# Kernel optimization log

Hardware: AMD Instinct MI355X
Metric: run time of the kernel (lower is better)

Reference implementation:

```python
import jax, jax.numpy as jnp
import numpy as np

N_HEADS = 16

def setup_inputs() -> dict:
    key = jax.random.key(0)
    k0, k1, k2 = jax.random.split(key, 3)
    B, T, C = 4, 2048, 1024
    x = jax.random.normal(k0, (B, T, C), dtype=jnp.float32)
    # nn.Linear params: y = x @ W.T + b
    w_qkv = jax.random.normal(k1, (3 * C, C), dtype=jnp.float32) * 0.02
    b_qkv = jnp.zeros((3 * C,), dtype=jnp.float32)
    w_proj = jax.random.normal(k2, (C, C), dtype=jnp.float32) * 0.02
    b_proj = jnp.zeros((C,), dtype=jnp.float32)
    return {"x": x, "w_qkv": w_qkv, "b_qkv": b_qkv, "w_proj": w_proj, "b_proj": b_proj}

def reference(x, w_qkv, b_qkv, w_proj, b_proj):
    B, T, C = x.shape
    H = N_HEADS
    hd = C // H
    qkv = x @ w_qkv.T + b_qkv                      # [B, T, 3C]
    q, k, v = jnp.split(qkv, 3, axis=-1)           # each [B, T, C]
    q = q.reshape(B, T, H, hd).transpose(0, 2, 1, 3)  # [B, H, T, hd]
    k = k.reshape(B, T, H, hd).transpose(0, 2, 1, 3)
    v = v.reshape(B, T, H, hd).transpose(0, 2, 1, 3)
    # note: original scales by emb_dim**-0.5 (C), not head_dim**-0.5
    wei = jnp.einsum("bhqd,bhkd->bhqk", q, k) * (C ** -0.5)  # [B, H, T, T]
    causal = jnp.tril(jnp.ones((T, T), dtype=bool))
    wei = jnp.where(causal, wei, -jnp.inf)
    att = jax.nn.softmax(wei, axis=-1)
    out = jnp.einsum("bhqk,bhkd->bhqd", att, v)    # [B, H, T, hd]
    out = out.transpose(0, 2, 1, 3).reshape(B, T, C)
    return out @ w_proj.T + b_proj
```

## Files before the change

### kernel.cpp

```cpp
#include <hip/hip_runtime.h>
#include <hip/hip_bf16.h>

typedef __bf16 bf16;
typedef __bf16 bf16x8 __attribute__((ext_vector_type(8)));
typedef __bf16 bf16x4 __attribute__((ext_vector_type(4)));
typedef float  f32x4  __attribute__((ext_vector_type(4)));

#define LDS_ASYNC16(g, l)                                            \
  __builtin_amdgcn_global_load_lds(                                  \
      (const __attribute__((address_space(1))) void*)(g),            \
      (__attribute__((address_space(3))) void*)(l), 16, 0, 0)

#define QSCALE 0.04508421995f

__global__ void cvt3_f32_bf16(const float* __restrict__ i0, bf16* __restrict__ o0, int n0,
                              const float* __restrict__ i1, bf16* __restrict__ o1, int n1,
                              const float* __restrict__ i2, bf16* __restrict__ o2, int n2) {
  int i = blockIdx.x * blockDim.x + threadIdx.x;
  const float* in;
  bf16* out;
  if (i < n0) {
    in = i0; out = o0;
  } else if (i < n0 + n1) {
    i -= n0; in = i1; out = o1;
  } else {
    i -= n0 + n1;
    if (i >= n2) return;
    in = i2; out = o2;
  }
  float4 v = ((const float4*)in)[i];
  bf16x4 o = {(bf16)v.x, (bf16)v.y, (bf16)v.z, (bf16)v.w};
  ((bf16x4*)out)[i] = o;
}

template <int MODE>
__global__ __launch_bounds__(512, 1) void gemm_bt(
    const bf16* __restrict__ A, const bf16* __restrict__ B,
    const float* __restrict__ bias, float* __restrict__ outf,
    bf16* __restrict__ oq, bf16* __restrict__ ok, bf16* __restrict__ ov,
    int M, int N, int K) {
  __shared__ __align__(16) bf16 As[2][256 * 64];
  __shared__ __align__(16) bf16 Bs[2][256 * 64];
  const int tid = threadIdx.x;
  const int wave = tid >> 6, lane = tid & 63;
  const int quad = lane >> 4, l15 = lane & 15, l7 = l15 & 7;
  const int wm = wave >> 2, wn = wave & 3;
  const int bm = blockIdx.x * 256, bn = blockIdx.y * 256;

  f32x4 acc[8][4] = {};

  const int csw = ((tid & 7) ^ ((tid >> 3) & 7)) * 8;
  const bf16* gA = A + (size_t)(bm + (tid >> 3)) * K + csw;
  const bf16* gB = B + (size_t)(bn + (tid >> 3)) * K + csw;
  const int KT = K >> 6;

#define ST_A(kt, cb, rb)                                               \
  LDS_ASYNC16(gA + (size_t)(rb) * K + (size_t)(kt) * 64,               \
              (char*)As + (cb) * 32768 + (rb) * 128 + wave * 1024)
#define ST_B(kt, cb, rb)                                               \
  LDS_ASYNC16(gB + (size_t)(rb) * K + (size_t)(kt) * 64,               \
              (char*)Bs + (cb) * 32768 + (rb) * 128 + wave * 1024)

  ST_A(0, 0, 0);   ST_A(0, 0, 128);
  ST_B(0, 0, 0);   ST_B(0, 0, 64);
  ST_A(0, 0, 64);  ST_A(0, 0, 192);
  ST_B(0, 0, 128); ST_B(0, 0, 192);
  ST_A(1, 1, 0);   ST_A(1, 1, 128);
  ST_B(1, 1, 0);   ST_B(1, 1, 64);
  ST_A(1, 1, 64);  ST_A(1, 1, 192);
  asm volatile("s_waitcnt vmcnt(6)" ::: "memory");
  __builtin_amdgcn_sched_barrier(0);
  __builtin_amdgcn_s_barrier();
  __builtin_amdgcn_sched_barrier(0);

  const int rowA = wm * 128 + l15;
  const int rowB = wn * 64 + l15;
  const int c0 = (quad ^ l7) * 16, c1 = ((4 + quad) ^ l7) * 16;

#pragma unroll 1
  for (int kt = 0; kt < KT; ++kt) {
    const int c = kt & 1;
    const char* bA = (const char*)As + c * 32768;
    const char* bB = (const char*)Bs + c * 32768;
    bf16x8 af[4][2], bg0[2][2], bg1[2][2];

#pragma unroll
    for (int mi = 0; mi < 4; ++mi) {
      af[mi][0] = *(const bf16x8*)(bA + (rowA + mi * 16) * 128 + c0);
      af[mi][1] = *(const bf16x8*)(bA + (rowA + mi * 16) * 128 + c1);
    }
#pragma unroll
    for (int ni = 0; ni < 2; ++ni) {
      bg0[ni][0] = *(const bf16x8*)(bB + (rowB + ni * 16) * 128 + c0);
      bg0[ni][1] = *(const bf16x8*)(bB + (rowB + ni * 16) * 128 + c1);
    }
    if (kt + 1 < KT) { ST_B(kt + 1, c ^ 1, 128); ST_B(kt + 1, c ^ 1, 192); }
    __builtin_amdgcn_sched_barrier(0);
    __builtin_amdgcn_s_barrier();
    asm volatile("s_waitcnt lgkmcnt(0)" ::: "memory");
    __builtin_amdgcn_sched_barrier(0);
    __builtin_amdgcn_s_setprio(1);
#pragma unroll
    for (int s = 0; s < 2; ++s)
#pragma unroll
      for (int mi = 0; mi < 4; ++mi)
#pragma unroll
        for (int ni = 0; ni < 2; ++ni)
          acc[mi][ni] = __builtin_amdgcn_mfma_f32_16x16x32_bf16(
              af[mi][s], bg0[ni][s], acc[mi][ni], 0, 0, 0);
    __builtin_amdgcn_s_setprio(0);
    __builtin_amdgcn_sched_barrier(0);
    __builtin_amdgcn_s_barrier();

#pragma unroll
    for (int ni = 0; ni < 2; ++ni) {
      bg1[ni][0] = *(const bf16x8*)(bB + (rowB + 32 + ni * 16) * 128 + c0);
      bg1[ni][1] = *(const bf16x8*)(bB + (rowB + 32 + ni * 16) * 128 + c1);
    }
    if (kt + 2 < KT) { ST_A(kt + 2, c, 0); ST_A(kt + 2, c, 128); }
    __builtin_amdgcn_sched_barrier(0);
    __builtin_amdgcn_s_barrier();
    asm volatile("s_waitcnt lgkmcnt(0)" ::: "memory");
    __builtin_amdgcn_sched_barrier(0);
    __builtin_amdgcn_s_setprio(1);
#pragma unroll
    for (int s = 0; s < 2; ++s)
#pragma unroll
      for (int mi = 0; mi < 4; ++mi)
#pragma unroll
        for (int ni = 0; ni < 2; ++ni)
          acc[mi][ni + 2] = __builtin_amdgcn_mfma_f32_16x16x32_bf16(
              af[mi][s], bg1[ni][s], acc[mi][ni + 2], 0, 0, 0);
    __builtin_amdgcn_s_setprio(0);
    __builtin_amdgcn_sched_barrier(0);
    __builtin_amdgcn_s_barrier();

#pragma unroll
    for (int mi = 0; mi < 4; ++mi) {
      af[mi][0] = *(const bf16x8*)(bA + (rowA + 64 + mi * 16) * 128 + c0);
      af[mi][1] = *(const bf16x8*)(bA + (rowA + 64 + mi * 16) * 128 + c1);
    }
    if (kt + 2 < KT) { ST_B(kt + 2, c, 0); ST_B(kt + 2, c, 64); }
    __builtin_amdgcn_sched_barrier(0);
    __builtin_amdgcn_s_barrier();
    asm volatile("s_waitcnt lgkmcnt(0)" ::: "memory");
    __builtin_amdgcn_sched_barrier(0);
    __builtin_amdgcn_s_setprio(1);
#pragma unroll
    for (int s = 0; s < 2; ++s)
#pragma unroll
      for (int mi = 0; mi < 4; ++mi)
#pragma unroll
        for (int ni = 0; ni < 2; ++ni)
          acc[mi + 4][ni + 2] = __builtin_amdgcn_mfma_f32_16x16x32_bf16(
              af[mi][s], bg1[ni][s], acc[mi + 4][ni + 2], 0, 0, 0);
    __builtin_amdgcn_s_setprio(0);
    __builtin_amdgcn_sched_barrier(0);
    __builtin_amdgcn_s_barrier();

    if (kt + 2 < KT) { ST_A(kt + 2, c, 64); ST_A(kt + 2, c, 192); }
    __builtin_amdgcn_sched_barrier(0);
    __builtin_amdgcn_s_barrier();
    __builtin_amdgcn_sched_barrier(0);
    __builtin_amdgcn_s_setprio(1);
#pragma unroll
    for (int s = 0; s < 2; ++s)
#pragma unroll
      for (int mi = 0; mi < 4; ++mi)
#pragma unroll
        for (int ni = 0; ni < 2; ++ni)
          acc[mi + 4][ni] = __builtin_amdgcn_mfma_f32_16x16x32_bf16(
              af[mi][s], bg0[ni][s], acc[mi + 4][ni], 0, 0, 0);
    __builtin_amdgcn_s_setprio(0);
    __builtin_amdgcn_sched_barrier(0);
    if (kt + 1 < KT) {
      if (kt + 2 < KT)
        asm volatile("s_waitcnt vmcnt(6)" ::: "memory");
      else
        asm volatile("s_waitcnt vmcnt(0)" ::: "memory");
      __builtin_amdgcn_sched_barrier(0);
      __builtin_amdgcn_s_barrier();
      __builtin_amdgcn_sched_barrier(0);
    }
  }
#undef ST_A
#undef ST_B

#pragma unroll
  for (int mi = 0; mi < 8; ++mi) {
    const int row0 = bm + wm * 128 + mi * 16 + quad * 4;
#pragma unroll
    for (int ni = 0; ni < 4; ++ni) {
      const int col = bn + wn * 64 + ni * 16 + l15;
      const float bv = bias[col];
      if (MODE == 0) {
#pragma unroll
        for (int r = 0; r < 4; ++r)
          outf[(size_t)(row0 + r) * N + col] = acc[mi][ni][r] + bv;
      } else {
        const int part = col >> 10;
        const int cn = col & 1023, h = cn >> 6, d = cn & 63;
        const int b = row0 >> 11, t0 = row0 & 2047;
        if (part == 2) {
          bf16x4 pk = {(bf16)(acc[mi][ni][0] + bv), (bf16)(acc[mi][ni][1] + bv),
                       (bf16)(acc[mi][ni][2] + bv), (bf16)(acc[mi][ni][3] + bv)};
          *(bf16x4*)(ov + ((size_t)(b * 16 + h) * 64 + d) * 2048 + t0) = pk;
        } else {
          const float sc = part ? 1.0f : QSCALE;
          bf16* dst = (part ? ok : oq) + ((size_t)(b * 16 + h) * 2048 + t0) * 64 + d;
#pragma unroll
          for (int r = 0; r < 4; ++r)
            dst[(size_t)r * 64] = (bf16)((acc[mi][ni][r] + bv) * sc);
        }
      }
    }
  }
}

__global__ __launch_bounds__(256) void flash_attn(
    const bf16* __restrict__ qb, const bf16* __restrict__ kb,
    const bf16* __restrict__ vt, bf16* __restrict__ ob) {
  constexpr int T = 2048;
  __shared__ bf16 Ks[2][64 * 72];
  __shared__ bf16 Vs[2][64 * 72];
  __shared__ float Ls[4][2][4][16];
  const int tid = threadIdx.x, wave = tid >> 6, lane = tid & 63;
  const int quad = lane >> 4, l15 = lane & 15;
  const int bh = blockIdx.x;
  const int b = bh >> 4, h = bh & 15;
  const bf16* qbase = qb + (size_t)bh * T * 64;
  const bf16* kbase = kb + (size_t)bh * T * 64;
  const bf16* vbase = vt + (size_t)bh * 64 * T;
  const int srow = tid >> 3, sc = (tid & 7) * 8;

  const int vp0 = (sc & ~31) | ((sc & 8) << 1) | ((sc & 16) >> 2);

  const int qt = 15 - (int)blockIdx.y;
  const int q0 = qt * 128 + wave * 32;

  bf16x8 qf[2][2];
#pragma unroll
  for (int qi = 0; qi < 2; ++qi)
#pragma unroll
    for (int ks = 0; ks < 2; ++ks)
      qf[qi][ks] = *(const bf16x8*)(qbase + (size_t)(q0 + qi * 16 + l15) * 64 +
                                    ks * 32 + quad * 8);

  f32x4 lsumv[2] = {};
  f32x4 oacc[2][4] = {};

  const int nkt = 2 * qt + 2;
  const int ktp = q0 >> 6;

  {
    uint4 k0 = *(const uint4*)(kbase + (size_t)srow * 64 + sc);
    uint4 k1 = *(const uint4*)(kbase + (size_t)(srow + 32) * 64 + sc);
    uint4 v0 = *(const uint4*)(vbase + (size_t)srow * T + sc);
    uint4 v1 = *(const uint4*)(vbase + (size_t)(srow + 32) * T + sc);
    *(uint4*)&Ks[0][srow * 72 + sc] = k0;
    *(uint4*)&Ks[0][(srow + 32) * 72 + sc] = k1;
    *(uint2*)&Vs[0][srow * 72 + vp0] = make_uint2(v0.x, v0.y);
    *(uint2*)&Vs[0][srow * 72 + vp0 + 8] = make_uint2(v0.z, v0.w);
    *(uint2*)&Vs[0][(srow + 32) * 72 + vp0] = make_uint2(v1.x, v1.y);
    *(uint2*)&Vs[0][(srow + 32) * 72 + vp0 + 8] = make_uint2(v1.z, v1.w);
  }

#pragma unroll 1
  for (int kt = 0; kt < nkt; ++kt) {
    __syncthreads();
    const int cur = kt & 1;
    const bool pre = (kt + 1) < nkt;
    uint4 pk0, pk1, pv0, pv1;
    if (pre) {
      const bf16* kp = kbase + (size_t)(kt + 1) * 64 * 64;
      const bf16* vp = vbase + (kt + 1) * 64;
      pk0 = *(const uint4*)(kp + (size_t)srow * 64 + sc);
      pk1 = *(const uint4*)(kp + (size_t)(srow + 32) * 64 + sc);
      pv0 = *(const uint4*)(vp + (size_t)srow * T + sc);
      pv1 = *(const uint4*)(vp + (size_t)(srow + 32) * T + sc);
    }
    if (kt <= ktp) {
      f32x4 st[4][2];
      __builtin_amdgcn_s_setprio(1);
#pragma unroll
      for (int ki = 0; ki < 4; ++ki) {
        bf16x8 kfa = *(const bf16x8*)&Ks[cur][(ki * 16 + l15) * 72 + quad * 8];
        bf16x8 kfb =
            *(const bf16x8*)&Ks[cur][(ki * 16 + l15) * 72 + 32 + quad * 8];
#pragma unroll
        for (int qi = 0; qi < 2; ++qi) {
          f32x4 a = {0.f, 0.f, 0.f, 0.f};
          a = __builtin_amdgcn_mfma_f32_16x16x32_bf16(kfa, qf[qi][0], a, 0, 0, 0);
          a = __builtin_amdgcn_mfma_f32_16x16x32_bf16(kfb, qf[qi][1], a, 0, 0, 0);
          st[ki][qi] = a;
        }
      }
      __builtin_amdgcn_s_setprio(0);
      if (kt == ktp) {
#pragma unroll
        for (int ki = 0; ki < 4; ++ki)
#pragma unroll
          for (int qi = 0; qi < 2; ++qi)
#pragma unroll
            for (int r = 0; r < 4; ++r) {
              const int kcol = kt * 64 + ki * 16 + quad * 4 + r;
              const int qrow = q0 + qi * 16 + l15;
              if (kcol > qrow) st[ki][qi][r] = -__builtin_inff();
            }
      }
#pragma unroll
      for (int ki = 0; ki < 4; ++ki)
#pragma unroll
        for (int qi = 0; qi < 2; ++qi) {
#pragma unroll
          for (int r = 0; r < 4; ++r)
            st[ki][qi][r] = __builtin_amdgcn_exp2f(st[ki][qi][r]);
          lsumv[qi] += st[ki][qi];
        }
      bf16x8 pa8[2][2];
#pragma unroll
      for (int ki2 = 0; ki2 < 2; ++ki2)
#pragma unroll
        for (int qi = 0; qi < 2; ++qi) {
          bf16x8 p;
#pragma unroll
          for (int r = 0; r < 4; ++r) {
            p[r] = (bf16)st[2 * ki2][qi][r];
            p[r + 4] = (bf16)st[2 * ki2 + 1][qi][r];
          }
          pa8[ki2][qi] = p;
        }
      __builtin_amdgcn_s_setprio(1);
#pragma unroll
      for (int di = 0; di < 4; ++di)
#pragma unroll
        for (int ki2 = 0; ki2 < 2; ++ki2) {
          bf16x8 vv = *(const bf16x8*)&Vs[cur][(di * 16 + l15) * 72 + ki2 * 32 +
                                              quad * 8];
#pragma unroll
          for (int qi = 0; qi < 2; ++qi)
            oacc[qi][di] = __builtin_amdgcn_mfma_f32_16x16x32_bf16(
                pa8[ki2][qi], vv, oacc[qi][di], 0, 0, 0);
        }
      __builtin_amdgcn_s_setprio(0);
    }
    if (pre) {
      const int nxt = cur ^ 1;
      *(uint4*)&Ks[nxt][srow * 72 + sc] = pk0;
      *(uint4*)&Ks[nxt][(srow + 32) * 72 + sc] = pk1;
      *(uint2*)&Vs[nxt][srow * 72 + vp0] = make_uint2(pv0.x, pv0.y);
      *(uint2*)&Vs[nxt][srow * 72 + vp0 + 8] = make_uint2(pv0.z, pv0.w);
      *(uint2*)&Vs[nxt][(srow + 32) * 72 + vp0] = make_uint2(pv1.x, pv1.y);
      *(uint2*)&Vs[nxt][(srow + 32) * 72 + vp0 + 8] = make_uint2(pv1.z, pv1.w);
    }
  }

#pragma unroll
  for (int qi = 0; qi < 2; ++qi)
    Ls[wave][qi][quad][l15] =
        lsumv[qi][0] + lsumv[qi][1] + lsumv[qi][2] + lsumv[qi][3];
#pragma unroll
  for (int qi = 0; qi < 2; ++qi)
#pragma unroll
    for (int r = 0; r < 4; ++r) {
      const int rloc = quad * 4 + r;
      const float l = Ls[wave][qi][0][rloc] + Ls[wave][qi][1][rloc] +
                      Ls[wave][qi][2][rloc] + Ls[wave][qi][3][rloc];
      const float inv = 1.f / l;
      const int t = q0 + qi * 16 + rloc;
#pragma unroll
      for (int di = 0; di < 4; ++di) {
        const int d = di * 16 + l15;
        ob[((size_t)b * 2048 + t) * 1024 + h * 64 + d] =
            (bf16)(oacc[qi][di][r] * inv);
      }
    }
}

extern "C" void kernel_launch(void* const* d_in, const int* in_sizes, int n_in,
                              void* d_out, int out_size, void* d_ws,
                              size_t ws_size, hipStream_t stream) {
  const float* x = (const float*)d_in[0];
  const float* w_qkv = (const float*)d_in[1];
  const float* b_qkv = (const float*)d_in[2];
  const float* w_proj = (const float*)d_in[3];
  const float* b_proj = (const float*)d_in[4];
  float* out = (float*)d_out;

  const int B = 4, T = 2048, C = 1024;
  const size_t nx = (size_t)B * T * C;

  char* ws = (char*)d_ws;
  bf16* xb = (bf16*)ws;      ws += nx * 2;
  bf16* wqkvb = (bf16*)ws;   ws += (size_t)3 * C * C * 2;
  bf16* wprojb = (bf16*)ws;  ws += (size_t)C * C * 2;
  bf16* qb = (bf16*)ws;      ws += nx * 2;
  bf16* kbuf = (bf16*)ws;    ws += nx * 2;
  bf16* vtb = (bf16*)ws;     ws += nx * 2;
  bf16* attb = (bf16*)ws;    ws += nx * 2;

  const int n0 = (int)(nx / 4), n1 = 3 * C * C / 4, n2 = C * C / 4;
  cvt3_f32_bf16<<<(n0 + n1 + n2 + 255) / 256, 256, 0, stream>>>(
      x, xb, n0, w_qkv, wqkvb, n1, w_proj, wprojb, n2);

  dim3 g1(32, 12);
  gemm_bt<1><<<g1, 512, 0, stream>>>(xb, wqkvb, b_qkv, nullptr, qb, kbuf, vtb,
                                     B * T, 3 * C, C);
  dim3 g2(64, 16);
  flash_attn<<<g2, 256, 0, stream>>>(qb, kbuf, vtb, attb);

  dim3 g3(32, 4);
  gemm_bt<0><<<g3, 512, 0, stream>>>(attb, wprojb, b_proj, out, nullptr,
                                     nullptr, nullptr, B * T, C, C);
}
```

Baseline: 259.8 us.

## Use smaller-tile multi-block GEMM for output projection; drop sched barriers

Adds a new 128x128-tile, 256-thread GEMM kernel with 4 blocks per CU and a simple double-buffered k-loop of 32, and uses it for the output projection. With the old 256x256 tiling that GEMM launched only 128 blocks on a machine with 256 CUs, so this is meant to fill the GPU and let blocks overlap. The original 8-wave kernel, renamed, still handles the QKV GEMM, with its sched_barrier fences removed so the compiler can interleave instructions more freely. The smaller tiles reread more operand data per FLOP, and dropping the fences may change how loads and MFMAs are interleaved.

```diff
diff --git a/kernel.cpp b/kernel.cpp
--- a/kernel.cpp
+++ b/kernel.cpp
@@ -34,7 +34,7 @@
 }
 
 template <int MODE>
-__global__ __launch_bounds__(512, 1) void gemm_bt(
+__global__ __launch_bounds__(512, 1) void gemm_bt8(
     const bf16* __restrict__ A, const bf16* __restrict__ B,
     const float* __restrict__ bias, float* __restrict__ outf,
     bf16* __restrict__ oq, bf16* __restrict__ ok, bf16* __restrict__ ov,
@@ -69,9 +69,7 @@
   ST_B(1, 1, 0);   ST_B(1, 1, 64);
   ST_A(1, 1, 64);  ST_A(1, 1, 192);
   asm volatile("s_waitcnt vmcnt(6)" ::: "memory");
-  __builtin_amdgcn_sched_barrier(0);
   __builtin_amdgcn_s_barrier();
-  __builtin_amdgcn_sched_barrier(0);
 
   const int rowA = wm * 128 + l15;
   const int rowB = wn * 64 + l15;
@@ -95,10 +93,8 @@
       bg0[ni][1] = *(const bf16x8*)(bB + (rowB + ni * 16) * 128 + c1);
     }
     if (kt + 1 < KT) { ST_B(kt + 1, c ^ 1, 128); ST_B(kt + 1, c ^ 1, 192); }
-    __builtin_amdgcn_sched_barrier(0);
     __builtin_amdgcn_s_barrier();
     asm volatile("s_waitcnt lgkmcnt(0)" ::: "memory");
-    __builtin_amdgcn_sched_barrier(0);
     __builtin_amdgcn_s_setprio(1);
 #pragma unroll
     for (int s = 0; s < 2; ++s)
@@ -109,7 +105,6 @@
           acc[mi][ni] = __builtin_amdgcn_mfma_f32_16x16x32_bf16(
               af[mi][s], bg0[ni][s], acc[mi][ni], 0, 0, 0);
     __builtin_amdgcn_s_setprio(0);
-    __builtin_amdgcn_sched_barrier(0);
     __builtin_amdgcn_s_barrier();
 
 #pragma unroll
@@ -118,10 +113,8 @@
       bg1[ni][1] = *(const bf16x8*)(bB + (rowB + 32 + ni * 16) * 128 + c1);
     }
     if (kt + 2 < KT) { ST_A(kt + 2, c, 0); ST_A(kt + 2, c, 128); }
-    __builtin_amdgcn_sched_barrier(0);
     __builtin_amdgcn_s_barrier();
     asm volatile("s_waitcnt lgkmcnt(0)" ::: "memory");
-    __builtin_amdgcn_sched_barrier(0);
     __builtin_amdgcn_s_setprio(1);
 #pragma unroll
     for (int s = 0; s < 2; ++s)
@@ -132,7 +125,6 @@
           acc[mi][ni + 2] = __builtin_amdgcn_mfma_f32_16x16x32_bf16(
               af[mi][s], bg1[ni][s], acc[mi][ni + 2], 0, 0, 0);
     __builtin_amdgcn_s_setprio(0);
-    __builtin_amdgcn_sched_barrier(0);
     __builtin_amdgcn_s_barrier();
 
 #pragma unroll
@@ -141,10 +133,8 @@
       af[mi][1] = *(const bf16x8*)(bA + (rowA + 64 + mi * 16) * 128 + c1);
     }
     if (kt + 2 < KT) { ST_B(kt + 2, c, 0); ST_B(kt + 2, c, 64); }
-    __builtin_amdgcn_sched_barrier(0);
     __builtin_amdgcn_s_barrier();
     asm volatile("s_waitcnt lgkmcnt(0)" ::: "memory");
-    __builtin_amdgcn_sched_barrier(0);
     __builtin_amdgcn_s_setprio(1);
 #pragma unroll
     for (int s = 0; s < 2; ++s)
@@ -155,13 +145,10 @@
           acc[mi + 4][ni + 2] = __builtin_amdgcn_mfma_f32_16x16x32_bf16(
               af[mi][s], bg1[ni][s], acc[mi + 4][ni + 2], 0, 0, 0);
     __builtin_amdgcn_s_setprio(0);
-    __builtin_amdgcn_sched_barrier(0);
     __builtin_amdgcn_s_barrier();
 
     if (kt + 2 < KT) { ST_A(kt + 2, c, 64); ST_A(kt + 2, c, 192); }
-    __builtin_amdgcn_sched_barrier(0);
-    __builtin_amdgcn_s_barrier();
-    __builtin_amdgcn_sched_barrier(0);
+    __builtin_amdgcn_s_barrier();
     __builtin_amdgcn_s_setprio(1);
 #pragma unroll
     for (int s = 0; s < 2; ++s)
@@ -172,15 +159,12 @@
           acc[mi + 4][ni] = __builtin_amdgcn_mfma_f32_16x16x32_bf16(
               af[mi][s], bg0[ni][s], acc[mi + 4][ni], 0, 0, 0);
     __builtin_amdgcn_s_setprio(0);
-    __builtin_amdgcn_sched_barrier(0);
     if (kt + 1 < KT) {
       if (kt + 2 < KT)
         asm volatile("s_waitcnt vmcnt(6)" ::: "memory");
       else
         asm volatile("s_waitcnt vmcnt(0)" ::: "memory");
-      __builtin_amdgcn_sched_barrier(0);
       __builtin_amdgcn_s_barrier();
-      __builtin_amdgcn_sched_barrier(0);
     }
   }
 #undef ST_A
@@ -192,6 +176,110 @@
 #pragma unroll
     for (int ni = 0; ni < 4; ++ni) {
       const int col = bn + wn * 64 + ni * 16 + l15;
+      const float bv = bias[col];
+      if (MODE == 0) {
+#pragma unroll
+        for (int r = 0; r < 4; ++r)
+          outf[(size_t)(row0 + r) * N + col] = acc[mi][ni][r] + bv;
+      } else {
+        const int part = col >> 10;
+        const int cn = col & 1023, h = cn >> 6, d = cn & 63;
+        const int b = row0 >> 11, t0 = row0 & 2047;
+        if (part == 2) {
+          bf16x4 pk = {(bf16)(acc[mi][ni][0] + bv), (bf16)(acc[mi][ni][1] + bv),
+                       (bf16)(acc[mi][ni][2] + bv), (bf16)(acc[mi][ni][3] + bv)};
+          *(bf16x4*)(ov + ((size_t)(b * 16 + h) * 64 + d) * 2048 + t0) = pk;
+        } else {
+          const float sc = part ? 1.0f : QSCALE;
+          bf16* dst = (part ? ok : oq) + ((size_t)(b * 16 + h) * 2048 + t0) * 64 + d;
+#pragma unroll
+          for (int r = 0; r < 4; ++r)
+            dst[(size_t)r * 64] = (bf16)((acc[mi][ni][r] + bv) * sc);
+        }
+      }
+    }
+  }
+}
+
+template <int MODE>
+__global__ __launch_bounds__(256, 4) void gemm_bt(
+    const bf16* __restrict__ A, const bf16* __restrict__ B,
+    const float* __restrict__ bias, float* __restrict__ outf,
+    bf16* __restrict__ oq, bf16* __restrict__ ok, bf16* __restrict__ ov,
+    int M, int N, int K) {
+  __shared__ __align__(16) bf16 As[2][128 * 32];
+  __shared__ __align__(16) bf16 Bs[2][128 * 32];
+  const int tid = threadIdx.x;
+  const int wave = tid >> 6, lane = tid & 63;
+  const int quad = lane >> 4, l15 = lane & 15;
+  const int bm = blockIdx.x * 128, bn = blockIdx.y * 128;
+  const int wrow = (wave >> 1) << 6, wcol = (wave & 1) << 6;
+
+  f32x4 acc[4][4] = {};
+
+  const int csw = ((tid & 3) ^ ((tid >> 3) & 3)) * 8;
+  const bf16* gA = A + (size_t)(bm + (tid >> 2)) * K + csw;
+  const bf16* gB = B + (size_t)(bn + (tid >> 2)) * K + csw;
+  char* lA = (char*)As + wave * 1024;
+  char* lB = (char*)Bs + wave * 1024;
+  const size_t K64 = (size_t)K * 64;
+  const int KT = K >> 5;
+
+#define ST(kt, cb) do {                                   \
+    const bf16* a_ = gA + (size_t)(kt) * 32;              \
+    const bf16* b_ = gB + (size_t)(kt) * 32;              \
+    LDS_ASYNC16(a_, lA + (cb) * 8192);                    \
+    LDS_ASYNC16(a_ + K64, lA + (cb) * 8192 + 4096);       \
+    LDS_ASYNC16(b_, lB + (cb) * 8192);                    \
+    LDS_ASYNC16(b_ + K64, lB + (cb) * 8192 + 4096);       \
+  } while (0)
+
+  ST(0, 0);
+  ST(1, 1);
+  asm volatile("s_waitcnt vmcnt(4)" ::: "memory");
+  __builtin_amdgcn_s_barrier();
+
+  const int gsw = (quad ^ ((l15 >> 1) & 3)) * 16;
+
+#pragma unroll 1
+  for (int kt = 0; kt < KT; ++kt) {
+    const int c = kt & 1;
+    const char* bA = (const char*)As + c * 8192;
+    const char* bB = (const char*)Bs + c * 8192;
+    bf16x8 af[4], bfr[4];
+#pragma unroll
+    for (int mi = 0; mi < 4; ++mi)
+      af[mi] = *(const bf16x8*)(bA + (wrow + mi * 16 + l15) * 64 + gsw);
+#pragma unroll
+    for (int ni = 0; ni < 4; ++ni)
+      bfr[ni] = *(const bf16x8*)(bB + (wcol + ni * 16 + l15) * 64 + gsw);
+    asm volatile("s_waitcnt lgkmcnt(0)" ::: "memory");
+    __builtin_amdgcn_s_barrier();
+    if (kt + 2 < KT) ST(kt + 2, c);
+    __builtin_amdgcn_s_setprio(1);
+#pragma unroll
+    for (int mi = 0; mi < 4; ++mi)
+#pragma unroll
+      for (int ni = 0; ni < 4; ++ni)
+        acc[mi][ni] = __builtin_amdgcn_mfma_f32_16x16x32_bf16(
+            af[mi], bfr[ni], acc[mi][ni], 0, 0, 0);
+    __builtin_amdgcn_s_setprio(0);
+    if (kt + 1 < KT) {
+      if (kt + 2 < KT)
+        asm volatile("s_waitcnt vmcnt(4)" ::: "memory");
+      else
+        asm volatile("s_waitcnt vmcnt(0)" ::: "memory");
+      __builtin_amdgcn_s_barrier();
+    }
+  }
+#undef ST
+
+#pragma unroll
+  for (int mi = 0; mi < 4; ++mi) {
+    const int row0 = bm + wrow + mi * 16 + quad * 4;
+#pragma unroll
+    for (int ni = 0; ni < 4; ++ni) {
+      const int col = bn + wcol + ni * 16 + l15;
       const float bv = bias[col];
       if (MODE == 0) {
 #pragma unroll
@@ -404,12 +492,12 @@
       x, xb, n0, w_qkv, wqkvb, n1, w_proj, wprojb, n2);
 
   dim3 g1(32, 12);
-  gemm_bt<1><<<g1, 512, 0, stream>>>(xb, wqkvb, b_qkv, nullptr, qb, kbuf, vtb,
-                                     B * T, 3 * C, C);
+  gemm_bt8<1><<<g1, 512, 0, stream>>>(xb, wqkvb, b_qkv, nullptr, qb, kbuf, vtb,
+                                      B * T, 3 * C, C);
   dim3 g2(64, 16);
   flash_attn<<<g2, 256, 0, stream>>>(qb, kbuf, vtb, attb);
 
-  dim3 g3(32, 4);
-  gemm_bt<0><<<g3, 512, 0, stream>>>(attb, wprojb, b_proj, out, nullptr,
+  dim3 g3(64, 8);
+  gemm_bt<0><<<g3, 256, 0, stream>>>(attb, wprojb, b_proj, out, nullptr,
                                      nullptr, nullptr, B * T, C, C);
 }
```

Measured after the change: 247.5 us. 4.7% less time.
